# Performance work log

Hardware: AMD Instinct MI355X
Metric: run time of the kernel (lower is better)

## Reference

```python
import jax, jax.numpy as jnp
import numpy as np

N, C, H, W = 64, 256, 28, 28
INTER = 128  # in_channels // reduction
STD = 0.01   # init std of the 1x1 convs


def setup_inputs() -> dict:
    key = jax.random.key(0)
    k_x, k_idx, k_wq, k_wv, k_lam = jax.random.split(key, 5)
    x = jax.random.normal(k_x, (N, C, H, W), dtype=jnp.float32)
    lam = jax.random.uniform(k_lam, (), dtype=jnp.float32)
    index = jax.random.randint(k_idx, (N,), 0, N)
    # query 1x1 conv (shared for q and k since x_qk_concat=False -> key is None)
    Wq = jax.random.normal(k_wq, (INTER, C), dtype=jnp.float32) * STD
    bq = jnp.zeros((INTER,), dtype=jnp.float32)
    # value 1x1 conv -> 1 channel
    Wv = jax.random.normal(k_wv, (1, C), dtype=jnp.float32) * STD
    bv = jnp.zeros((1,), dtype=jnp.float32)
    return {"x": x, "lam": lam, "index": index, "Wq": Wq, "bq": bq,
            "Wv": Wv, "bv": bv, "scale_factor": 8}


def _conv1x1(x, w, b):
    # x: [n,c,h,w], w: [o,c], b: [o] -> [n,o,h,w]
    return jnp.einsum('nchw,oc->nohw', x, w) + b[None, :, None, None]


def reference(x, lam, index, Wq, bq, Wv, bv, scale_factor):
    n, c, h, w = x.shape
    hw = h * w
    x_lam = x               # [n,c,h,w]
    x_lam_ = x[index]       # shuffled pair
    # value: 1x1 conv to 1 channel -> [n, hw, 1]
    v = _conv1x1(x_lam_, Wv, bv).reshape(n, 1, hw).transpose(0, 2, 1)
    # query / key share the same conv (key is None when x_qk_concat=False)
    q = _conv1x1(x_lam, Wq, bq).reshape(n, INTER, hw).transpose(0, 2, 1)  # [n,hw,inter]
    k = _conv1x1(x_lam_, Wq, bq).reshape(n, INTER, hw)                    # [n,inter,hw]
    # embedded gaussian similarity, forced fp32, scaled by sqrt(inter)
    scores = jnp.einsum('nqc,nck->nqk', q.astype(jnp.float32), k.astype(jnp.float32))
    scores = scores / jnp.float32(np.sqrt(INTER))
    pw = jax.nn.softmax(scores, axis=-1)  # [n,hw,hw]
    mask = jnp.einsum('nqk,nko->nqo', pw, v.astype(jnp.float32)).reshape(n, 1, h, w)
    # bilinear upsample (align_corners=False semantics) then sigmoid
    mask = jax.image.resize(mask, (n, 1, h * scale_factor, w * scale_factor),
                            method='bilinear')
    mask = jax.nn.sigmoid(mask)
    # results['mask'] = cat([1 - m, m], dim=1)
    return jnp.concatenate([1.0 - mask, mask], axis=1)
```

## Files before the change

kernel.cpp:

```cpp
#include <hip/hip_runtime.h>
#include <math.h>

#define NB    64
#define CIN   256
#define HH    28
#define WW    28
#define HW    784
#define INTER 128

typedef __bf16 bf16x8 __attribute__((ext_vector_type(8)));
typedef float  f32x4  __attribute__((ext_vector_type(4)));

#define SCALE 0.35709723f

#define GLB(p) ((const __attribute__((address_space(1))) void*)(p))
#define LDSP(p) ((__attribute__((address_space(3))) void*)(p))

__device__ __forceinline__ unsigned int bfbits(float f) {
    unsigned int u = __builtin_bit_cast(unsigned int, f);
    return (u + 0x7fffu + ((u >> 16) & 1u)) >> 16;
}

__global__ __launch_bounds__(256) void initw_kernel(
    const float* __restrict__ Wq, unsigned short* __restrict__ Wbh)
{
    const int e  = blockIdx.x * 256 + threadIdx.x;
    const int j  = e & 7;
    const int l  = (e >> 3) & 63;
    const int it = (e >> 9) & 7;
    const int s  = e >> 12;
    const int i  = it * 16 + (l & 15);
    const int c  = s * 32 + ((l >> 4) & 3) * 8 + j;
    Wbh[e] = (unsigned short)bfbits(Wq[i * CIN + c] * SCALE);
}

__global__ __launch_bounds__(256, 5) void proj_kernel(
    const float* __restrict__ x,
    const unsigned short* __restrict__ Wfh,
    const float* __restrict__ bq,
    const float* __restrict__ Wv, const float* __restrict__ bv,
    unsigned short* __restrict__ Yb, float* __restrict__ vAll)
{
    __shared__ float          Xs [2][32 * 64];
    __shared__ unsigned short Whs[2][4096];

    const int ptile = blockIdx.x;
    const int n     = blockIdx.y;
    const int t     = threadIdx.x;
    const int l     = t & 63;
    const int w     = t >> 6;
    const int pl    = l & 15;
    const int g     = l >> 4;
    const int p0    = ptile * 64;

    const float* xn = x + (size_t)n * (CIN * HW);

    const int kk    = pl ^ (w << 2);
    const int psrc  = min(p0 + kk * 4, HW - 4);

    const int slot  = ((w * 16 + pl) >> 2) ^ (g << 2);
    const int rbyte = slot * 4 + (pl & 3);

    f32x4 acc[8];
#pragma unroll
    for (int it = 0; it < 8; ++it) acc[it] = (f32x4){0.f, 0.f, 0.f, 0.f};
    float vpart = 0.0f;

#pragma unroll
    for (int q = 0; q < 2; ++q) {
        const int rt = w * 8 + q * 4 + g;
        __builtin_amdgcn_global_load_lds(GLB(xn + (size_t)rt * HW + psrc),
                                         LDSP(&Xs[0][(w * 8 + q * 4) * 64]), 16, 0, 0);
        const int chunk = (w * 2 + q) * 512;
        __builtin_amdgcn_global_load_lds(GLB(Wfh + chunk + l * 8),
                                         LDSP(&Whs[0][chunk]), 16, 0, 0);
    }
    __syncthreads();

    int cur = 0;
    for (int s = 0; s < 8; ++s) {
        if (s < 7) {
#pragma unroll
            for (int q = 0; q < 2; ++q) {
                const int rt = w * 8 + q * 4 + g;
                __builtin_amdgcn_global_load_lds(
                    GLB(xn + (size_t)((s + 1) * 32 + rt) * HW + psrc),
                    LDSP(&Xs[cur ^ 1][(w * 8 + q * 4) * 64]), 16, 0, 0);
                const int chunk = (w * 2 + q) * 512;
                __builtin_amdgcn_global_load_lds(
                    GLB(Wfh + (s + 1) * 4096 + chunk + l * 8),
                    LDSP(&Whs[cur ^ 1][chunk]), 16, 0, 0);
            }
        }

        float xv[8];
#pragma unroll
        for (int j = 0; j < 8; ++j)
            xv[j] = Xs[cur][(g * 8 + j) * 64 + rbyte];

        const float4 wv0 = *(const float4*)(Wv + s * 32 + g * 8);
        const float4 wv1 = *(const float4*)(Wv + s * 32 + g * 8 + 4);
        vpart = fmaf(xv[0], wv0.x, fmaf(xv[1], wv0.y,
                fmaf(xv[2], wv0.z, fmaf(xv[3], wv0.w, vpart))));
        vpart = fmaf(xv[4], wv1.x, fmaf(xv[5], wv1.y,
                fmaf(xv[6], wv1.z, fmaf(xv[7], wv1.w, vpart))));

        bf16x8 ah;
#pragma unroll
        for (int j = 0; j < 8; ++j) ah[j] = (__bf16)xv[j];

#pragma unroll
        for (int it = 0; it < 8; ++it) {
            const bf16x8 wh = *(const bf16x8*)&Whs[cur][it * 512 + l * 8];
            acc[it] = __builtin_amdgcn_mfma_f32_16x16x32_bf16(ah, wh, acc[it], 0, 0, 0);
        }

        __syncthreads();
        cur ^= 1;
    }

    const int p0w = p0 + w * 16;

    vpart += __shfl_xor(vpart, 16);
    vpart += __shfl_xor(vpart, 32);
    if (g == 0 && p0w + pl < HW)
        vAll[n * HW + p0w + pl] = vpart + bv[0];

#pragma unroll
    for (int it = 0; it < 8; ++it) {
        const int i = it * 16 + pl;
        const float bb = bq[i] * SCALE;
#pragma unroll
        for (int r = 0; r < 4; ++r) {
            const int pr = p0w + g * 4 + r;
            if (pr < HW)
                Yb[((size_t)n * HW + pr) * INTER + i] =
                    (unsigned short)bfbits(acc[it][r] + bb);
        }
    }
}

__global__ __launch_bounds__(256) void attn_kernel(
    const unsigned short* __restrict__ Yb, const float* __restrict__ vAll,
    const int* __restrict__ index, float* __restrict__ maskbuf)
{
    __shared__ __align__(16) unsigned char ldsraw[52224 + 3584];
    float* red = (float*)(ldsraw + 52224);

    const int n   = blockIdx.x;
    const int qt  = blockIdx.y;
    const int q0  = qt * 112;
    const int t   = threadIdx.x;
    const int l   = t & 63;
    const int w   = t >> 6;
    const int idx = index[n];

    const unsigned short* Qg = Yb + (size_t)n   * (HW * INTER);
    const unsigned short* Kg = Yb + (size_t)idx * (HW * INTER);
    const float*          Vg = vAll + (size_t)idx * HW;

    const int ql = l & 15;
    const int g  = l >> 4;
    const int wbase = w * 13056;

    bf16x8 qf[7][4];
#pragma unroll
    for (int qg = 0; qg < 7; ++qg) {
        const int qrow = q0 + qg * 16 + ql;
#pragma unroll
        for (int ic = 0; ic < 4; ++ic)
            qf[qg][ic] = *(const bf16x8*)(Qg + (size_t)qrow * INTER + ic * 32 + g * 8);
    }

    float ll[7] = {0.f, 0.f, 0.f, 0.f, 0.f, 0.f, 0.f};
    float oo[7] = {0.f, 0.f, 0.f, 0.f, 0.f, 0.f, 0.f};

    const int NT = (w == 0) ? 13 : 12;

#define ISSUE(kt_, slot_)                                                   \
    {                                                                       \
        const int sb = wbase + (slot_) * 4352;                              \
        _Pragma("unroll")                                                   \
        for (int j = 0; j < 4; ++j) {                                       \
            const int row = (j << 2) + (l >> 4);                            \
            const int c   = (l & 15) ^ row;                                 \
            const unsigned short* src =                                     \
                Kg + (size_t)((kt_) * 64 + w * 16 + row) * INTER + c * 8;   \
            __builtin_amdgcn_global_load_lds(GLB(src),                      \
                LDSP(ldsraw + sb + j * 1024 + l * 16), 16, 0, 0);           \
        }                                                                   \
        __builtin_amdgcn_global_load_lds(                                   \
            GLB(Vg + (kt_) * 64 + w * 16 + (l & 15)),                       \
            LDSP(ldsraw + sb + 4096 + l * 4), 4, 0, 0);                     \
    }

    ISSUE(0, 0)
    ISSUE(1, 1)
    ISSUE(2, 2)

    int slot = 0;
    for (int kt = 0; kt < NT; ++kt) {
        if (kt + 2 < NT)      asm volatile("s_waitcnt vmcnt(10)" ::: "memory");
        else if (kt + 1 < NT) asm volatile("s_waitcnt vmcnt(5)"  ::: "memory");
        else                  asm volatile("s_waitcnt vmcnt(0)"  ::: "memory");
        __builtin_amdgcn_sched_barrier(0);

        const int sb = wbase + slot * 4352;
        bf16x8 af[4];
#pragma unroll
        for (int ic = 0; ic < 4; ++ic) {
            const int s_ = (ic * 4 + g) ^ ql;
            af[ic] = *(const bf16x8*)(ldsraw + sb + ql * 256 + s_ * 16);
        }
        const float4 vv = *(const float4*)(ldsraw + sb + 4096 + g * 16);

#pragma unroll
        for (int qg = 0; qg < 7; ++qg) {
            f32x4 acc = (f32x4){0.f, 0.f, 0.f, 0.f};
#pragma unroll
            for (int ic = 0; ic < 4; ++ic)
                acc = __builtin_amdgcn_mfma_f32_16x16x32_bf16(
                    af[ic], qf[qg][ic], acc, 0, 0, 0);
            const float e0 = exp2f(acc[0]);
            const float e1 = exp2f(acc[1]);
            const float e2 = exp2f(acc[2]);
            const float e3 = exp2f(acc[3]);
            ll[qg] += (e0 + e1) + (e2 + e3);
            oo[qg] = fmaf(e0, vv.x, fmaf(e1, vv.y,
                     fmaf(e2, vv.z, fmaf(e3, vv.w, oo[qg]))));
        }

        if (kt + 3 < NT) ISSUE(kt + 3, slot)

        slot = (slot == 2) ? 0 : slot + 1;
    }
#undef ISSUE

#pragma unroll
    for (int qg = 0; qg < 7; ++qg) {
        ll[qg] += __shfl_xor(ll[qg], 16); ll[qg] += __shfl_xor(ll[qg], 32);
        oo[qg] += __shfl_xor(oo[qg], 16); oo[qg] += __shfl_xor(oo[qg], 32);
    }
    if (g == 0) {
#pragma unroll
        for (int qg = 0; qg < 7; ++qg) {
            red[(0 * 4 + w) * 112 + qg * 16 + ql] = ll[qg];
            red[(1 * 4 + w) * 112 + qg * 16 + ql] = oo[qg];
        }
    }
    __syncthreads();
    if (t < 112) {
        const float L = red[0 * 448 + 0 * 112 + t] + red[0 * 448 + 1 * 112 + t]
                      + red[0 * 448 + 2 * 112 + t] + red[0 * 448 + 3 * 112 + t];
        const float O = red[1 * 448 + 0 * 112 + t] + red[1 * 448 + 1 * 112 + t]
                      + red[1 * 448 + 2 * 112 + t] + red[1 * 448 + 3 * 112 + t];
        maskbuf[n * HW + q0 + t] = O / L;
    }
}

__global__ __launch_bounds__(256) void upsample_kernel(
    const float* __restrict__ maskbuf, float* __restrict__ out)
{
    const int gid = blockIdx.x * 256 + threadIdx.x;
    const int n  = gid / (224 * 56);
    const int r  = gid - n * (224 * 56);
    const int oy = r / 56;
    const int xq = r - oy * 56;

    const float iy = (oy + 0.5f) * 0.125f - 0.5f;
    const int   y0 = (int)floorf(iy);
    const float fy = iy - (float)y0;
    const int y0c = max(y0, 0), y1c = min(y0 + 1, HH - 1);
    const float* mrow = maskbuf + n * HW;

    float res[4];
#pragma unroll
    for (int j = 0; j < 4; ++j) {
        const int   ox = (xq << 2) + j;
        const float ix = (ox + 0.5f) * 0.125f - 0.5f;
        const int   x0 = (int)floorf(ix);
        const float fx = ix - (float)x0;
        const int x0c = max(x0, 0), x1c = min(x0 + 1, WW - 1);
        const float v00 = mrow[y0c * WW + x0c], v01 = mrow[y0c * WW + x1c];
        const float v10 = mrow[y1c * WW + x0c], v11 = mrow[y1c * WW + x1c];
        const float m = (v00 * (1.0f - fx) + v01 * fx) * (1.0f - fy)
                      + (v10 * (1.0f - fx) + v11 * fx) * fy;
        res[j] = 1.0f / (1.0f + __expf(-m));
    }

    float4 pos = make_float4(res[0], res[1], res[2], res[3]);
    float4 neg = make_float4(1.0f - res[0], 1.0f - res[1],
                             1.0f - res[2], 1.0f - res[3]);
    const size_t base = (size_t)n * 2 * 50176 + (size_t)oy * 224 + (xq << 2);
    *(float4*)(out + base)         = neg;
    *(float4*)(out + base + 50176) = pos;
}

extern "C" void kernel_launch(void* const* d_in, const int* in_sizes, int n_in,
                              void* d_out, int out_size, void* d_ws, size_t ws_size,
                              hipStream_t stream) {
    const float* x     = (const float*)d_in[0];
    const int*   index = (const int*)d_in[2];
    const float* Wq    = (const float*)d_in[3];
    const float* bq    = (const float*)d_in[4];
    const float* Wv    = (const float*)d_in[5];
    const float* bv    = (const float*)d_in[6];

    float* out = (float*)d_out;
    unsigned short* Yb  = (unsigned short*)d_out;
    unsigned short* Wbh = Yb + (size_t)NB * HW * INTER;
    float* vAll  = (float*)d_ws;
    float* maskb = vAll + NB * HW;

    initw_kernel<<<128, 256, 0, stream>>>(Wq, Wbh);
    proj_kernel<<<dim3(13, NB), 256, 0, stream>>>(x, Wbh, bq, Wv, bv, Yb, vAll);
    attn_kernel<<<dim3(NB, 7), 256, 0, stream>>>(Yb, vAll, index, maskb);
    upsample_kernel<<<3136, 256, 0, stream>>>(maskb, out);
}
```

Measured before the change: 62.62 us.

## Split attention keys across two blocks and merge partial sums in upsample

The attention kernel now splits the 13 key tiles across a new grid z-dimension of two blocks. Each block writes partial softmax denominators and numerators, and the upsample kernel combines them when it reads each mask value. This doubles the attention grid from 448 to 896 blocks to fill the GPU's compute units better. It also cuts the prefetch ring from three to two LDS slots, which lowers LDS use per block, and it swaps the projection grid order so the batch index varies fastest. The costs are that each block reloads its Q fragments, partial results take extra global traffic, and upsample does redundant loads and divides.

Result: slower. 80.43 us (+28.4%).

```diff
diff --git a/kernel.cpp b/kernel.cpp
--- a/kernel.cpp
+++ b/kernel.cpp
@@ -44,8 +44,8 @@
     __shared__ float          Xs [2][32 * 64];
     __shared__ unsigned short Whs[2][4096];
 
-    const int ptile = blockIdx.x;
-    const int n     = blockIdx.y;
+    const int n     = blockIdx.x;
+    const int ptile = blockIdx.y;
     const int t     = threadIdx.x;
     const int l     = t & 63;
     const int w     = t >> 6;
@@ -142,13 +142,14 @@
 
 __global__ __launch_bounds__(256) void attn_kernel(
     const unsigned short* __restrict__ Yb, const float* __restrict__ vAll,
-    const int* __restrict__ index, float* __restrict__ maskbuf)
+    const int* __restrict__ index, float* __restrict__ Lp, float* __restrict__ Op)
 {
-    __shared__ __align__(16) unsigned char ldsraw[52224 + 3584];
-    float* red = (float*)(ldsraw + 52224);
+    __shared__ __align__(16) unsigned char ldsraw[34816 + 3584];
+    float* red = (float*)(ldsraw + 34816);
 
     const int n   = blockIdx.x;
     const int qt  = blockIdx.y;
+    const int z   = blockIdx.z;
     const int q0  = qt * 112;
     const int t   = threadIdx.x;
     const int l   = t & 63;
@@ -161,7 +162,7 @@
 
     const int ql = l & 15;
     const int g  = l >> 4;
-    const int wbase = w * 13056;
+    const int wbase = w * 8704;
 
     bf16x8 qf[7][4];
 #pragma unroll
@@ -175,9 +176,10 @@
     float ll[7] = {0.f, 0.f, 0.f, 0.f, 0.f, 0.f, 0.f};
     float oo[7] = {0.f, 0.f, 0.f, 0.f, 0.f, 0.f, 0.f};
 
-    const int NT = (w == 0) ? 13 : 12;
-
-#define ISSUE(kt_, slot_)                                                   \
+    const int kt0 = z * 6;
+    const int NTl = (z == 0) ? 6 : ((w == 0) ? 7 : 6);
+
+#define ISSUE(kti_, slot_)                                                  \
     {                                                                       \
         const int sb = wbase + (slot_) * 4352;                              \
         _Pragma("unroll")                                                   \
@@ -185,24 +187,22 @@
             const int row = (j << 2) + (l >> 4);                            \
             const int c   = (l & 15) ^ row;                                 \
             const unsigned short* src =                                     \
-                Kg + (size_t)((kt_) * 64 + w * 16 + row) * INTER + c * 8;   \
+                Kg + (size_t)((kt0 + (kti_)) * 64 + w * 16 + row) * INTER + c * 8; \
             __builtin_amdgcn_global_load_lds(GLB(src),                      \
                 LDSP(ldsraw + sb + j * 1024 + l * 16), 16, 0, 0);           \
         }                                                                   \
         __builtin_amdgcn_global_load_lds(                                   \
-            GLB(Vg + (kt_) * 64 + w * 16 + (l & 15)),                       \
+            GLB(Vg + (kt0 + (kti_)) * 64 + w * 16 + (l & 15)),              \
             LDSP(ldsraw + sb + 4096 + l * 4), 4, 0, 0);                     \
     }
 
     ISSUE(0, 0)
     ISSUE(1, 1)
-    ISSUE(2, 2)
 
     int slot = 0;
-    for (int kt = 0; kt < NT; ++kt) {
-        if (kt + 2 < NT)      asm volatile("s_waitcnt vmcnt(10)" ::: "memory");
-        else if (kt + 1 < NT) asm volatile("s_waitcnt vmcnt(5)"  ::: "memory");
-        else                  asm volatile("s_waitcnt vmcnt(0)"  ::: "memory");
+    for (int kt = 0; kt < NTl; ++kt) {
+        if (kt + 1 < NTl) asm volatile("s_waitcnt vmcnt(5)" ::: "memory");
+        else              asm volatile("s_waitcnt vmcnt(0)" ::: "memory");
         __builtin_amdgcn_sched_barrier(0);
 
         const int sb = wbase + slot * 4352;
@@ -230,9 +230,9 @@
                      fmaf(e2, vv.z, fmaf(e3, vv.w, oo[qg]))));
         }
 
-        if (kt + 3 < NT) ISSUE(kt + 3, slot)
-
-        slot = (slot == 2) ? 0 : slot + 1;
+        if (kt + 2 < NTl) ISSUE(kt + 2, slot)
+
+        slot ^= 1;
     }
 #undef ISSUE
 
@@ -254,12 +254,14 @@
                       + red[0 * 448 + 2 * 112 + t] + red[0 * 448 + 3 * 112 + t];
         const float O = red[1 * 448 + 0 * 112 + t] + red[1 * 448 + 1 * 112 + t]
                       + red[1 * 448 + 2 * 112 + t] + red[1 * 448 + 3 * 112 + t];
-        maskbuf[n * HW + q0 + t] = O / L;
+        Lp[(size_t)z * (NB * HW) + n * HW + q0 + t] = L;
+        Op[(size_t)z * (NB * HW) + n * HW + q0 + t] = O;
     }
 }
 
 __global__ __launch_bounds__(256) void upsample_kernel(
-    const float* __restrict__ maskbuf, float* __restrict__ out)
+    const float* __restrict__ Lp, const float* __restrict__ Op,
+    float* __restrict__ out)
 {
     const int gid = blockIdx.x * 256 + threadIdx.x;
     const int n  = gid / (224 * 56);
@@ -271,7 +273,9 @@
     const int   y0 = (int)floorf(iy);
     const float fy = iy - (float)y0;
     const int y0c = max(y0, 0), y1c = min(y0 + 1, HH - 1);
-    const float* mrow = maskbuf + n * HW;
+    const int base_n = n * HW;
+
+#define MVAL(p) ((Op[(p)] + Op[NB * HW + (p)]) / (Lp[(p)] + Lp[NB * HW + (p)]))
 
     float res[4];
 #pragma unroll
@@ -281,12 +285,15 @@
         const int   x0 = (int)floorf(ix);
         const float fx = ix - (float)x0;
         const int x0c = max(x0, 0), x1c = min(x0 + 1, WW - 1);
-        const float v00 = mrow[y0c * WW + x0c], v01 = mrow[y0c * WW + x1c];
-        const float v10 = mrow[y1c * WW + x0c], v11 = mrow[y1c * WW + x1c];
+        const float v00 = MVAL(base_n + y0c * WW + x0c);
+        const float v01 = MVAL(base_n + y0c * WW + x1c);
+        const float v10 = MVAL(base_n + y1c * WW + x0c);
+        const float v11 = MVAL(base_n + y1c * WW + x1c);
         const float m = (v00 * (1.0f - fx) + v01 * fx) * (1.0f - fy)
                       + (v10 * (1.0f - fx) + v11 * fx) * fy;
         res[j] = 1.0f / (1.0f + __expf(-m));
     }
+#undef MVAL
 
     float4 pos = make_float4(res[0], res[1], res[2], res[3]);
     float4 neg = make_float4(1.0f - res[0], 1.0f - res[1],
@@ -309,11 +316,12 @@
     float* out = (float*)d_out;
     unsigned short* Yb  = (unsigned short*)d_out;
     unsigned short* Wbh = Yb + (size_t)NB * HW * INTER;
-    float* vAll  = (float*)d_ws;
-    float* maskb = vAll + NB * HW;
+    float* vAll = (float*)d_ws;
+    float* Lp   = vAll + NB * HW;
+    float* Op   = Lp + 2 * NB * HW;
 
     initw_kernel<<<128, 256, 0, stream>>>(Wq, Wbh);
-    proj_kernel<<<dim3(13, NB), 256, 0, stream>>>(x, Wbh, bq, Wv, bv, Yb, vAll);
-    attn_kernel<<<dim3(NB, 7), 256, 0, stream>>>(Yb, vAll, index, maskb);
-    upsample_kernel<<<3136, 256, 0, stream>>>(maskb, out);
-}
+    proj_kernel<<<dim3(NB, 13), 256, 0, stream>>>(x, Wbh, bq, Wv, bv, Yb, vAll);
+    attn_kernel<<<dim3(NB, 7, 2), 256, 0, stream>>>(Yb, vAll, index, Lp, Op);
+    upsample_kernel<<<3136, 256, 0, stream>>>(Lp, Op, out);
+}
```
